# Performance work log

Measured on AMD Instinct MI355X. Metric: run time of the kernel, lower is better.

The kernel has to match this reference:

```python
import jax, jax.numpy as jnp
import numpy as np

B, T, D, HS = 8, 2048, 768, 64  # batch, seq, n_embd, head_size


def setup_inputs() -> dict:
    key = jax.random.key(0)
    kx, kq, kk, kv = jax.random.split(key, 4)
    scale = 1.0 / np.sqrt(D)
    return {
        "x": jax.random.normal(kx, (B, T, D), dtype=jnp.float32),
        "Wq": jax.random.normal(kq, (D, HS), dtype=jnp.float32) * scale,
        "Wk": jax.random.normal(kk, (D, HS), dtype=jnp.float32) * scale,
        "Wv": jax.random.normal(kv, (D, HS), dtype=jnp.float32) * scale,
    }


def reference(x, Wq, Wk, Wv):
    # q,k,v: [B,T,HS]
    q = jnp.einsum("btd,dh->bth", x, Wq)
    k = jnp.einsum("btd,dh->bth", x, Wk)
    v = jnp.einsum("btd,dh->bth", x, Wv)
    hs = k.shape[-1]
    # scaled scores: [B,T,T]
    wei = jnp.einsum("bth,bsh->bts", q, k) * (hs ** -0.5)
    # causal mask (lower-triangular keeps, upper -> -inf)
    causal = jnp.tril(jnp.ones((x.shape[1], x.shape[1]), dtype=bool))
    wei = jnp.where(causal[None, :, :], wei, -jnp.inf)
    wei = jax.nn.softmax(wei, axis=-1)
    return jnp.einsum("bts,bsh->bth", wei, v)
```

## Files before the change

kernel.cpp:

```cpp
#include <hip/hip_runtime.h>

typedef float  f32x4  __attribute__((ext_vector_type(4)));
typedef short  short8 __attribute__((ext_vector_type(8)));
typedef short  short4_ __attribute__((ext_vector_type(4)));

constexpr int Bb = 8, T = 2048, D = 768, HS = 64;
constexpr int BT = Bb * T;
constexpr int QT = T / 64;
constexpr int PSTRIDE = 64 * 64 + 128;

__device__ __forceinline__ short f2bf(float f) {
    unsigned u = __builtin_bit_cast(unsigned, f);
    unsigned r = (u + 0x7FFFu + ((u >> 16) & 1u)) >> 16;
    return (short)r;
}

__device__ __forceinline__ void gld_lds16(const short* g, short* l) {
    __builtin_amdgcn_global_load_lds(
        (const __attribute__((address_space(1))) unsigned int*)g,
        (__attribute__((address_space(3))) unsigned int*)l, 16, 0, 0);
}

__global__ __launch_bounds__(256) void wt_kernel(const float* __restrict__ Wq,
                                                 const float* __restrict__ Wk,
                                                 const float* __restrict__ Wv,
                                                 short* __restrict__ Wt) {
    int n = blockIdx.x;
    const float* W = (n < 64) ? Wq : (n < 128) ? Wk : Wv;
    int c = n & 63;
    for (int kk = threadIdx.x; kk < D; kk += 256)
        Wt[n * D + kk] = f2bf(W[kk * HS + c]);
}

__global__ __launch_bounds__(512) void qkv_proj(const float* __restrict__ x,
                                                const short* __restrict__ Wt,
                                                short* __restrict__ qws,
                                                short* __restrict__ kws,
                                                short* __restrict__ vtg) {
    __shared__ alignas(16) short xs[2][64 * 72];
    __shared__ alignas(16) short wtile[2][192 * 64];

    const int tid  = threadIdx.x;
    const int lane = tid & 63, w = tid >> 6;
    const int lo   = lane & 15, hi = lane >> 4;
    const int wr   = w >> 2, wc = w & 3;
    const int row0 = blockIdx.x * 64;
    const int b    = row0 >> 11, t0 = row0 & 2047;

    const int xr0 = tid >> 4, xsg = tid & 15;
    const float* xsrc0 = &x[(size_t)(row0 + xr0) * D + xsg * 4];
    const float* xsrc1 = &x[(size_t)(row0 + 32 + xr0) * D + xsg * 4];

    f32x4 acc[6];
#pragma unroll
    for (int j = 0; j < 6; j++) acc[j] = f32x4{0.f, 0.f, 0.f, 0.f};

#define STAGE(bb, kc)                                                          \
    {                                                                          \
        _Pragma("unroll")                                                      \
        for (int it = 0; it < 3; it++) {                                       \
            int ci = it * 512 + w * 64 + lane;                                 \
            int n = ci >> 3, seg = ci & 7;                                     \
            gld_lds16(&Wt[(size_t)n * D + (kc) * 64 + ((seg ^ (n & 7)) << 3)], \
                      &wtile[bb][(it * 512 + w * 64) * 8]);                    \
        }                                                                      \
        float4 f0 = *reinterpret_cast<const float4*>(xsrc0 + (kc) * 64);       \
        float4 f1 = *reinterpret_cast<const float4*>(xsrc1 + (kc) * 64);       \
        short4_ h0, h1;                                                        \
        h0[0] = f2bf(f0.x); h0[1] = f2bf(f0.y); h0[2] = f2bf(f0.z); h0[3] = f2bf(f0.w); \
        h1[0] = f2bf(f1.x); h1[1] = f2bf(f1.y); h1[2] = f2bf(f1.z); h1[3] = f2bf(f1.w); \
        *reinterpret_cast<short4_*>(&xs[bb][xr0 * 72 + xsg * 4]) = h0;         \
        *reinterpret_cast<short4_*>(&xs[bb][(32 + xr0) * 72 + xsg * 4]) = h1;  \
    }

    STAGE(0, 0);
    __syncthreads();

    for (int kc = 0; kc < 12; kc++) {
        const int bb = kc & 1;
        if (kc + 1 < 12) STAGE(bb ^ 1, kc + 1);

#pragma unroll
        for (int m = 0; m < 2; m++) {
            const int ar = (wr * 32 + m * 16 + lo) * 72;
            short8 a0 = *reinterpret_cast<const short8*>(&xs[bb][ar + hi * 8]);
            short8 a1 = *reinterpret_cast<const short8*>(&xs[bb][ar + 32 + hi * 8]);
#pragma unroll
            for (int j = 0; j < 3; j++) {
                const int row = wc * 48 + j * 16 + lo;
                const int rx  = (row & 7) << 3;
                short8 b0 = *reinterpret_cast<const short8*>(
                    &wtile[bb][row * 64 + ((hi << 3) ^ rx)]);
                short8 b1 = *reinterpret_cast<const short8*>(
                    &wtile[bb][row * 64 + (((hi + 4) << 3) ^ rx)]);
                acc[m * 3 + j] = __builtin_amdgcn_mfma_f32_16x16x32_bf16(a0, b0, acc[m * 3 + j], 0, 0, 0);
                acc[m * 3 + j] = __builtin_amdgcn_mfma_f32_16x16x32_bf16(a1, b1, acc[m * 3 + j], 0, 0, 0);
            }
        }
        __syncthreads();
    }
#undef STAGE

#pragma unroll
    for (int m = 0; m < 2; m++) {
        const int orow = row0 + wr * 32 + m * 16 + hi * 4;
#pragma unroll
        for (int j = 0; j < 3; j++) {
            const int cb = wc * 48 + j * 16;
            const f32x4 a = acc[m * 3 + j];
            if (cb < 64) {
#pragma unroll
                for (int r = 0; r < 4; r++)
                    qws[(size_t)(orow + r) * HS + cb + lo] = f2bf(a[r] * 0.125f);
            } else if (cb < 128) {
#pragma unroll
                for (int r = 0; r < 4; r++)
                    kws[(size_t)(orow + r) * HS + cb - 64 + lo] = f2bf(a[r]);
            } else {
                short4_ pv;
#pragma unroll
                for (int r = 0; r < 4; r++) pv[r] = f2bf(a[r]);
                *reinterpret_cast<short4_*>(
                    &vtg[((size_t)b * 64 + cb - 128 + lo) * T + t0 + wr * 32 + m * 16 + hi * 4]) = pv;
            }
        }
    }
}

__global__ __launch_bounds__(256) void attn(const short* __restrict__ qg,
                                            const short* __restrict__ kg,
                                            const short* __restrict__ vtg,
                                            float* __restrict__ part, int S) {
    __shared__ short ks[2][64 * 64];
    __shared__ short vts[2][64 * 64];
    __shared__ short ps[4][16 * 64];

    const int tid  = threadIdx.x;
    const int lane = tid & 63, w = tid >> 6;
    const int lo   = lane & 15, hi = lane >> 4;
    const int bid  = blockIdx.x;
    const int per_b = QT * S;
    const int b    = bid / per_b;
    const int r2   = bid % per_b;
    const int qt   = 31 - (r2 / S);
    const int c    = r2 % S;
    const int nkt  = qt + 1;
    const int base = nkt / S, rem = nkt % S;
    const int niter = base + (c < rem ? 1 : 0);
    const int kt0   = c * base + (c < rem ? c : rem);
    float* pout = part + (size_t)((b * QT + qt) * S + c) * PSTRIDE;

    float m_[4], l_[4];
    f32x4 oacc[4];
#pragma unroll
    for (int r = 0; r < 4; r++) { m_[r] = -1e30f; l_[r] = 0.0f; }
#pragma unroll
    for (int i = 0; i < 4; i++) oacc[i] = f32x4{0.f, 0.f, 0.f, 0.f};

    if (niter > 0) {
        const int qrow = qt * 64 + w * 16 + lo;
        const size_t qbase = ((size_t)b * T + qrow) * HS;
        short8 qa0 = *reinterpret_cast<const short8*>(&qg[qbase + hi * 8]);
        short8 qa1 = *reinterpret_cast<const short8*>(&qg[qbase + 32 + hi * 8]);

        const int srow = tid >> 2, scs = tid & 3, r7 = srow & 7;
        const int w0 = srow * 64 + (((scs * 2)     ^ r7) << 3);
        const int w1 = srow * 64 + (((scs * 2 + 1) ^ r7) << 3);
        const size_t kgoff = (size_t)b * T * HS;
        const size_t vgoff = ((size_t)b * 64 + srow) * T;

        short8 ka, kb2, va, vb;
        {
            const short* kp = &kg[kgoff + (size_t)(kt0 * 64 + srow) * HS + scs * 16];
            ka = *reinterpret_cast<const short8*>(kp);
            kb2 = *reinterpret_cast<const short8*>(kp + 8);
            const short* vp = &vtg[vgoff + kt0 * 64 + scs * 16];
            va = *reinterpret_cast<const short8*>(vp);
            vb = *reinterpret_cast<const short8*>(vp + 8);
        }
        *reinterpret_cast<short8*>(&ks[0][w0])  = ka;
        *reinterpret_cast<short8*>(&ks[0][w1])  = kb2;
        *reinterpret_cast<short8*>(&vts[0][w0]) = va;
        *reinterpret_cast<short8*>(&vts[0][w1]) = vb;

        int cur = 0;
        for (int i = 0; i < niter; i++) {
            const int kt = kt0 + i;
            if (i + 1 < niter) {
                const short* kp = &kg[kgoff + (size_t)((kt + 1) * 64 + srow) * HS + scs * 16];
                ka = *reinterpret_cast<const short8*>(kp);
                kb2 = *reinterpret_cast<const short8*>(kp + 8);
                const short* vp = &vtg[vgoff + (kt + 1) * 64 + scs * 16];
                va = *reinterpret_cast<const short8*>(vp);
                vb = *reinterpret_cast<const short8*>(vp + 8);
            }
            __syncthreads();

            f32x4 sacc[4];
#pragma unroll
            for (int nt = 0; nt < 4; nt++) sacc[nt] = f32x4{0.f, 0.f, 0.f, 0.f};
            __builtin_amdgcn_s_setprio(1);
#pragma unroll
            for (int nt = 0; nt < 4; nt++) {
                const int row = nt * 16 + lo, rr = row & 7;
                short8 b0 = *reinterpret_cast<const short8*>(
                    &ks[cur][row * 64 + ((hi ^ rr) << 3)]);
                short8 b1 = *reinterpret_cast<const short8*>(
                    &ks[cur][row * 64 + (((hi + 4) ^ rr) << 3)]);
                sacc[nt] = __builtin_amdgcn_mfma_f32_16x16x32_bf16(qa0, b0, sacc[nt], 0, 0, 0);
                sacc[nt] = __builtin_amdgcn_mfma_f32_16x16x32_bf16(qa1, b1, sacc[nt], 0, 0, 0);
            }
            __builtin_amdgcn_s_setprio(0);

            if (kt == qt) {
#pragma unroll
                for (int nt = 0; nt < 4; nt++)
#pragma unroll
                    for (int r = 0; r < 4; r++)
                        if (nt * 16 + lo > w * 16 + hi * 4 + r) sacc[nt][r] = -1e30f;
            }

#pragma unroll
            for (int r = 0; r < 4; r++) {
                float t0m = fmaxf(fmaxf(sacc[0][r], sacc[1][r]),
                                  fmaxf(sacc[2][r], sacc[3][r]));
#pragma unroll
                for (int off = 1; off < 16; off <<= 1) t0m = fmaxf(t0m, __shfl_xor(t0m, off));
                float mnew = fmaxf(m_[r], t0m);
                float corr = __expf(m_[r] - mnew);
                float psum = 0.0f;
#pragma unroll
                for (int nt = 0; nt < 4; nt++) {
                    float p = __expf(sacc[nt][r] - mnew);
                    sacc[nt][r] = p;
                    psum += p;
                }
#pragma unroll
                for (int off = 1; off < 16; off <<= 1) psum += __shfl_xor(psum, off);
                l_[r] = l_[r] * corr + psum;
                m_[r] = mnew;
#pragma unroll
                for (int nt = 0; nt < 4; nt++) oacc[nt][r] *= corr;
            }

#pragma unroll
            for (int nt = 0; nt < 4; nt++)
#pragma unroll
                for (int r = 0; r < 4; r++) {
                    const int qr = hi * 4 + r;
                    const int seg = nt * 2 + (lo >> 3);
                    ps[w][qr * 64 + ((seg ^ (qr & 7)) << 3) + (lo & 7)] = f2bf(sacc[nt][r]);
                }

            const int pl7 = lo & 7;
            short8 pa0 = *reinterpret_cast<const short8*>(
                &ps[w][lo * 64 + ((hi ^ pl7) << 3)]);
            short8 pa1 = *reinterpret_cast<const short8*>(
                &ps[w][lo * 64 + (((hi + 4) ^ pl7) << 3)]);
            __builtin_amdgcn_s_setprio(1);
#pragma unroll
            for (int nt = 0; nt < 4; nt++) {
                const int row = nt * 16 + lo, rr = row & 7;
                short8 b0 = *reinterpret_cast<const short8*>(
                    &vts[cur][row * 64 + ((hi ^ rr) << 3)]);
                short8 b1 = *reinterpret_cast<const short8*>(
                    &vts[cur][row * 64 + (((hi + 4) ^ rr) << 3)]);
                oacc[nt] = __builtin_amdgcn_mfma_f32_16x16x32_bf16(pa0, b0, oacc[nt], 0, 0, 0);
                oacc[nt] = __builtin_amdgcn_mfma_f32_16x16x32_bf16(pa1, b1, oacc[nt], 0, 0, 0);
            }
            __builtin_amdgcn_s_setprio(0);

            if (i + 1 < niter) {
                *reinterpret_cast<short8*>(&ks[cur ^ 1][w0])  = ka;
                *reinterpret_cast<short8*>(&ks[cur ^ 1][w1])  = kb2;
                *reinterpret_cast<short8*>(&vts[cur ^ 1][w0]) = va;
                *reinterpret_cast<short8*>(&vts[cur ^ 1][w1]) = vb;
            }
            cur ^= 1;
        }
    }

#pragma unroll
    for (int nt = 0; nt < 4; nt++)
#pragma unroll
        for (int r = 0; r < 4; r++)
            pout[(w * 16 + hi * 4 + r) * 64 + nt * 16 + lo] = oacc[nt][r];
    if (lo == 0) {
#pragma unroll
        for (int r = 0; r < 4; r++) {
            const int row = w * 16 + hi * 4 + r;
            pout[4096 + row] = m_[r];
            pout[4160 + row] = l_[r];
        }
    }
}

__global__ __launch_bounds__(256) void combine(const float* __restrict__ part,
                                               float* __restrict__ out, int S) {
    const int bid = blockIdx.x;
    const int b = bid >> 5, qt = bid & 31;
    const float* p = part + (size_t)bid * S * PSTRIDE;
    const int row = threadIdx.x >> 2, cs = threadIdx.x & 3;

    float mv[4], lv[4], av[4];
    float M = -1e30f;
    for (int s = 0; s < S; s++) {
        mv[s] = p[(size_t)s * PSTRIDE + 4096 + row];
        lv[s] = p[(size_t)s * PSTRIDE + 4160 + row];
        M = fmaxf(M, mv[s]);
    }
    float den = 0.0f;
    for (int s = 0; s < S; s++) { av[s] = __expf(mv[s] - M); den += lv[s] * av[s]; }
    float inv = 1.0f / den;

    float* o = out + ((size_t)b * T + qt * 64 + row) * HS + cs * 16;
#pragma unroll
    for (int i = 0; i < 4; i++) {
        float4 res = make_float4(0.f, 0.f, 0.f, 0.f);
        for (int s = 0; s < S; s++) {
            float4 v = *reinterpret_cast<const float4*>(
                p + (size_t)s * PSTRIDE + row * 64 + cs * 16 + i * 4);
            res.x += v.x * av[s]; res.y += v.y * av[s];
            res.z += v.z * av[s]; res.w += v.w * av[s];
        }
        res.x *= inv; res.y *= inv; res.z *= inv; res.w *= inv;
        *reinterpret_cast<float4*>(o + i * 4) = res;
    }
}

extern "C" void kernel_launch(void* const* d_in, const int* in_sizes, int n_in,
                              void* d_out, int out_size, void* d_ws, size_t ws_size,
                              hipStream_t stream) {
    const float* x  = (const float*)d_in[0];
    const float* Wq = (const float*)d_in[1];
    const float* Wk = (const float*)d_in[2];
    const float* Wv = (const float*)d_in[3];
    float* out = (float*)d_out;

    short* ws   = (short*)d_ws;
    short* qws  = ws;
    short* kws  = qws + (size_t)BT * HS;
    short* vtws = kws + (size_t)BT * HS;
    short* Wt   = vtws + (size_t)BT * HS;
    float* part = (float*)(Wt + (size_t)192 * D);

    const size_t fixed = (size_t)3 * BT * HS * 2 + (size_t)192 * D * 2;
    int S = 4;
    while (S > 1 && fixed + (size_t)Bb * QT * S * PSTRIDE * 4 > ws_size) S >>= 1;

    wt_kernel<<<192, 256, 0, stream>>>(Wq, Wk, Wv, Wt);
    qkv_proj<<<BT / 64, 512, 0, stream>>>(x, Wt, qws, kws, vtws);
    attn<<<Bb * QT * S, 256, 0, stream>>>(qws, kws, vtws, part, S);
    combine<<<Bb * QT, 256, 0, stream>>>(part, out, S);
}
```

Baseline: 63.42 us.

## Halve QKV projection row tile and load x directly into registers

The QKV projection block now covers 32 rows instead of 64, which doubles the grid. Each wave loads its x fragment straight from global memory into registers, with a one-step prefetch, and converts it to bf16 there, so the shared-memory x tile is gone. A launch-bounds occupancy hint is added. The aim is more parallelism and less LDS traffic in the projection. In exchange, each W tile loaded into LDS is reused across half as many rows, so total W traffic doubles.

```diff
diff --git a/kernel.cpp b/kernel.cpp
--- a/kernel.cpp
+++ b/kernel.cpp
@@ -32,30 +32,27 @@
         Wt[n * D + kk] = f2bf(W[kk * HS + c]);
 }
 
-__global__ __launch_bounds__(512) void qkv_proj(const float* __restrict__ x,
-                                                const short* __restrict__ Wt,
-                                                short* __restrict__ qws,
-                                                short* __restrict__ kws,
-                                                short* __restrict__ vtg) {
-    __shared__ alignas(16) short xs[2][64 * 72];
+__global__ __launch_bounds__(512, 4) void qkv_proj(const float* __restrict__ x,
+                                                   const short* __restrict__ Wt,
+                                                   short* __restrict__ qws,
+                                                   short* __restrict__ kws,
+                                                   short* __restrict__ vtg) {
     __shared__ alignas(16) short wtile[2][192 * 64];
 
     const int tid  = threadIdx.x;
     const int lane = tid & 63, w = tid >> 6;
     const int lo   = lane & 15, hi = lane >> 4;
     const int wr   = w >> 2, wc = w & 3;
-    const int row0 = blockIdx.x * 64;
+    const int row0 = blockIdx.x * 32;
     const int b    = row0 >> 11, t0 = row0 & 2047;
 
-    const int xr0 = tid >> 4, xsg = tid & 15;
-    const float* xsrc0 = &x[(size_t)(row0 + xr0) * D + xsg * 4];
-    const float* xsrc1 = &x[(size_t)(row0 + 32 + xr0) * D + xsg * 4];
-
-    f32x4 acc[6];
-#pragma unroll
-    for (int j = 0; j < 6; j++) acc[j] = f32x4{0.f, 0.f, 0.f, 0.f};
-
-#define STAGE(bb, kc)                                                          \
+    const float* xrow = &x[(size_t)(row0 + wr * 16 + lo) * D];
+
+    f32x4 acc[3];
+#pragma unroll
+    for (int j = 0; j < 3; j++) acc[j] = f32x4{0.f, 0.f, 0.f, 0.f};
+
+#define STAGE_W(bb, kc)                                                        \
     {                                                                          \
         _Pragma("unroll")                                                      \
         for (int it = 0; it < 3; it++) {                                       \
@@ -64,65 +61,74 @@
             gld_lds16(&Wt[(size_t)n * D + (kc) * 64 + ((seg ^ (n & 7)) << 3)], \
                       &wtile[bb][(it * 512 + w * 64) * 8]);                    \
         }                                                                      \
-        float4 f0 = *reinterpret_cast<const float4*>(xsrc0 + (kc) * 64);       \
-        float4 f1 = *reinterpret_cast<const float4*>(xsrc1 + (kc) * 64);       \
-        short4_ h0, h1;                                                        \
-        h0[0] = f2bf(f0.x); h0[1] = f2bf(f0.y); h0[2] = f2bf(f0.z); h0[3] = f2bf(f0.w); \
-        h1[0] = f2bf(f1.x); h1[1] = f2bf(f1.y); h1[2] = f2bf(f1.z); h1[3] = f2bf(f1.w); \
-        *reinterpret_cast<short4_*>(&xs[bb][xr0 * 72 + xsg * 4]) = h0;         \
-        *reinterpret_cast<short4_*>(&xs[bb][(32 + xr0) * 72 + xsg * 4]) = h1;  \
-    }
-
-    STAGE(0, 0);
+    }
+
+    STAGE_W(0, 0);
+    float4 cur[4], nxt[4];
+    cur[0] = *reinterpret_cast<const float4*>(xrow + hi * 8);
+    cur[1] = *reinterpret_cast<const float4*>(xrow + hi * 8 + 4);
+    cur[2] = *reinterpret_cast<const float4*>(xrow + 32 + hi * 8);
+    cur[3] = *reinterpret_cast<const float4*>(xrow + 32 + hi * 8 + 4);
     __syncthreads();
 
+#pragma unroll
     for (int kc = 0; kc < 12; kc++) {
         const int bb = kc & 1;
-        if (kc + 1 < 12) STAGE(bb ^ 1, kc + 1);
-
-#pragma unroll
-        for (int m = 0; m < 2; m++) {
-            const int ar = (wr * 32 + m * 16 + lo) * 72;
-            short8 a0 = *reinterpret_cast<const short8*>(&xs[bb][ar + hi * 8]);
-            short8 a1 = *reinterpret_cast<const short8*>(&xs[bb][ar + 32 + hi * 8]);
-#pragma unroll
-            for (int j = 0; j < 3; j++) {
-                const int row = wc * 48 + j * 16 + lo;
-                const int rx  = (row & 7) << 3;
-                short8 b0 = *reinterpret_cast<const short8*>(
-                    &wtile[bb][row * 64 + ((hi << 3) ^ rx)]);
-                short8 b1 = *reinterpret_cast<const short8*>(
-                    &wtile[bb][row * 64 + (((hi + 4) << 3) ^ rx)]);
-                acc[m * 3 + j] = __builtin_amdgcn_mfma_f32_16x16x32_bf16(a0, b0, acc[m * 3 + j], 0, 0, 0);
-                acc[m * 3 + j] = __builtin_amdgcn_mfma_f32_16x16x32_bf16(a1, b1, acc[m * 3 + j], 0, 0, 0);
-            }
+        if (kc + 1 < 12) {
+            STAGE_W(bb ^ 1, kc + 1);
+            const float* xp = xrow + (kc + 1) * 64;
+            nxt[0] = *reinterpret_cast<const float4*>(xp + hi * 8);
+            nxt[1] = *reinterpret_cast<const float4*>(xp + hi * 8 + 4);
+            nxt[2] = *reinterpret_cast<const float4*>(xp + 32 + hi * 8);
+            nxt[3] = *reinterpret_cast<const float4*>(xp + 32 + hi * 8 + 4);
+        }
+
+        short8 a0, a1;
+#pragma unroll
+        for (int e = 0; e < 4; e++) {
+            a0[e]     = f2bf(cur[0][e]);
+            a0[e + 4] = f2bf(cur[1][e]);
+            a1[e]     = f2bf(cur[2][e]);
+            a1[e + 4] = f2bf(cur[3][e]);
+        }
+
+#pragma unroll
+        for (int j = 0; j < 3; j++) {
+            const int row = wc * 48 + j * 16 + lo;
+            const int rx  = (row & 7) << 3;
+            short8 b0 = *reinterpret_cast<const short8*>(
+                &wtile[bb][row * 64 + ((hi << 3) ^ rx)]);
+            short8 b1 = *reinterpret_cast<const short8*>(
+                &wtile[bb][row * 64 + (((hi + 4) << 3) ^ rx)]);
+            acc[j] = __builtin_amdgcn_mfma_f32_16x16x32_bf16(a0, b0, acc[j], 0, 0, 0);
+            acc[j] = __builtin_amdgcn_mfma_f32_16x16x32_bf16(a1, b1, acc[j], 0, 0, 0);
         }
         __syncthreads();
-    }
-#undef STAGE
-
-#pragma unroll
-    for (int m = 0; m < 2; m++) {
-        const int orow = row0 + wr * 32 + m * 16 + hi * 4;
-#pragma unroll
-        for (int j = 0; j < 3; j++) {
-            const int cb = wc * 48 + j * 16;
-            const f32x4 a = acc[m * 3 + j];
-            if (cb < 64) {
-#pragma unroll
-                for (int r = 0; r < 4; r++)
-                    qws[(size_t)(orow + r) * HS + cb + lo] = f2bf(a[r] * 0.125f);
-            } else if (cb < 128) {
-#pragma unroll
-                for (int r = 0; r < 4; r++)
-                    kws[(size_t)(orow + r) * HS + cb - 64 + lo] = f2bf(a[r]);
-            } else {
-                short4_ pv;
-#pragma unroll
-                for (int r = 0; r < 4; r++) pv[r] = f2bf(a[r]);
-                *reinterpret_cast<short4_*>(
-                    &vtg[((size_t)b * 64 + cb - 128 + lo) * T + t0 + wr * 32 + m * 16 + hi * 4]) = pv;
-            }
+
+#pragma unroll
+        for (int i = 0; i < 4; i++) cur[i] = nxt[i];
+    }
+#undef STAGE_W
+
+    const int orow = row0 + wr * 16 + hi * 4;
+#pragma unroll
+    for (int j = 0; j < 3; j++) {
+        const int cb = wc * 48 + j * 16;
+        const f32x4 a = acc[j];
+        if (cb < 64) {
+#pragma unroll
+            for (int r = 0; r < 4; r++)
+                qws[(size_t)(orow + r) * HS + cb + lo] = f2bf(a[r] * 0.125f);
+        } else if (cb < 128) {
+#pragma unroll
+            for (int r = 0; r < 4; r++)
+                kws[(size_t)(orow + r) * HS + cb - 64 + lo] = f2bf(a[r]);
+        } else {
+            short4_ pv;
+#pragma unroll
+            for (int r = 0; r < 4; r++) pv[r] = f2bf(a[r]);
+            *reinterpret_cast<short4_*>(
+                &vtg[((size_t)b * 64 + cb - 128 + lo) * T + t0 + wr * 16 + hi * 4]) = pv;
         }
     }
 }
@@ -349,7 +355,7 @@
     while (S > 1 && fixed + (size_t)Bb * QT * S * PSTRIDE * 4 > ws_size) S >>= 1;
 
     wt_kernel<<<192, 256, 0, stream>>>(Wq, Wk, Wv, Wt);
-    qkv_proj<<<BT / 64, 512, 0, stream>>>(x, Wt, qws, kws, vtws);
+    qkv_proj<<<BT / 32, 512, 0, stream>>>(x, Wt, qws, kws, vtws);
     attn<<<Bb * QT * S, 256, 0, stream>>>(qws, kws, vtws, part, S);
     combine<<<Bb * QT, 256, 0, stream>>>(part, out, S);
 }
```

New measurement: 75.43 us. +18.9%, slower.

## Process two key tiles per attention iteration and stage V transpose through LDS

Applied to the files above, without the earlier changes.

The attention loop now handles two 64-key tiles per iteration, with double-buffered LDS holding both tiles. This halves the number of block barriers and online-softmax rescale steps per key, and shares one max and sum reduction across 128 keys. Separately, the QKV projection writes V into shared memory and then stores the transposed V with coalesced 16-byte writes instead of scattered 8-byte writes. The trade-off is double the LDS footprint and more registers in attention, which may lower occupancy.

```diff
diff --git a/kernel.cpp b/kernel.cpp
--- a/kernel.cpp
+++ b/kernel.cpp
@@ -39,6 +39,7 @@
                                                 short* __restrict__ vtg) {
     __shared__ alignas(16) short xs[2][64 * 72];
     __shared__ alignas(16) short wtile[2][192 * 64];
+    __shared__ alignas(16) short vs[64 * 72];
 
     const int tid  = threadIdx.x;
     const int lane = tid & 63, w = tid >> 6;
@@ -104,6 +105,7 @@
 #pragma unroll
     for (int m = 0; m < 2; m++) {
         const int orow = row0 + wr * 32 + m * 16 + hi * 4;
+        const int trow = wr * 32 + m * 16 + hi * 4;
 #pragma unroll
         for (int j = 0; j < 3; j++) {
             const int cb = wc * 48 + j * 16;
@@ -117,13 +119,20 @@
                 for (int r = 0; r < 4; r++)
                     kws[(size_t)(orow + r) * HS + cb - 64 + lo] = f2bf(a[r]);
             } else {
-                short4_ pv;
-#pragma unroll
-                for (int r = 0; r < 4; r++) pv[r] = f2bf(a[r]);
-                *reinterpret_cast<short4_*>(
-                    &vtg[((size_t)b * 64 + cb - 128 + lo) * T + t0 + wr * 32 + m * 16 + hi * 4]) = pv;
+#pragma unroll
+                for (int r = 0; r < 4; r++)
+                    vs[(trow + r) * 72 + cb - 128 + lo] = f2bf(a[r]);
             }
         }
+    }
+    __syncthreads();
+    {
+        const int h = tid >> 3, ts = tid & 7;
+        short8 tmp;
+#pragma unroll
+        for (int e = 0; e < 8; e++) tmp[e] = vs[(ts * 8 + e) * 72 + h];
+        *reinterpret_cast<short8*>(
+            &vtg[((size_t)b * 64 + h) * T + t0 + ts * 8]) = tmp;
     }
 }
 
@@ -131,9 +140,9 @@
                                             const short* __restrict__ kg,
                                             const short* __restrict__ vtg,
                                             float* __restrict__ part, int S) {
-    __shared__ short ks[2][64 * 64];
-    __shared__ short vts[2][64 * 64];
-    __shared__ short ps[4][16 * 64];
+    __shared__ short ks[2][2][64 * 64];
+    __shared__ short vts[2][2][64 * 64];
+    __shared__ short ps[4][16 * 128];
 
     const int tid  = threadIdx.x;
     const int lane = tid & 63, w = tid >> 6;
@@ -169,71 +178,112 @@
         const size_t kgoff = (size_t)b * T * HS;
         const size_t vgoff = ((size_t)b * 64 + srow) * T;
 
-        short8 ka, kb2, va, vb;
-        {
-            const short* kp = &kg[kgoff + (size_t)(kt0 * 64 + srow) * HS + scs * 16];
-            ka = *reinterpret_cast<const short8*>(kp);
-            kb2 = *reinterpret_cast<const short8*>(kp + 8);
-            const short* vp = &vtg[vgoff + kt0 * 64 + scs * 16];
-            va = *reinterpret_cast<const short8*>(vp);
-            vb = *reinterpret_cast<const short8*>(vp + 8);
-        }
-        *reinterpret_cast<short8*>(&ks[0][w0])  = ka;
-        *reinterpret_cast<short8*>(&ks[0][w1])  = kb2;
-        *reinterpret_cast<short8*>(&vts[0][w0]) = va;
-        *reinterpret_cast<short8*>(&vts[0][w1]) = vb;
-
+#define LOADT(kt64, KA, KB, VA, VB)                                            \
+    {                                                                          \
+        const short* kp = &kg[kgoff + (size_t)((kt64) * 64 + srow) * HS + scs * 16]; \
+        KA = *reinterpret_cast<const short8*>(kp);                             \
+        KB = *reinterpret_cast<const short8*>(kp + 8);                         \
+        const short* vp = &vtg[vgoff + (kt64) * 64 + scs * 16];                \
+        VA = *reinterpret_cast<const short8*>(vp);                             \
+        VB = *reinterpret_cast<const short8*>(vp + 8);                         \
+    }
+#define STORET(buf, half, KA, KB, VA, VB)                                      \
+    {                                                                          \
+        *reinterpret_cast<short8*>(&ks[buf][half][w0])  = KA;                  \
+        *reinterpret_cast<short8*>(&ks[buf][half][w1])  = KB;                  \
+        *reinterpret_cast<short8*>(&vts[buf][half][w0]) = VA;                  \
+        *reinterpret_cast<short8*>(&vts[buf][half][w1]) = VB;                  \
+    }
+
+        short8 kA0, kB0, vA0, vB0, kA1, kB1, vA1, vB1;
+        LOADT(kt0, kA0, kB0, vA0, vB0);
+        if (1 < niter) LOADT(kt0 + 1, kA1, kB1, vA1, vB1);
+        STORET(0, 0, kA0, kB0, vA0, vB0);
+        if (1 < niter) STORET(0, 1, kA1, kB1, vA1, vB1);
+
+        const int npair = (niter + 1) >> 1;
         int cur = 0;
-        for (int i = 0; i < niter; i++) {
-            const int kt = kt0 + i;
-            if (i + 1 < niter) {
-                const short* kp = &kg[kgoff + (size_t)((kt + 1) * 64 + srow) * HS + scs * 16];
-                ka = *reinterpret_cast<const short8*>(kp);
-                kb2 = *reinterpret_cast<const short8*>(kp + 8);
-                const short* vp = &vtg[vgoff + (kt + 1) * 64 + scs * 16];
-                va = *reinterpret_cast<const short8*>(vp);
-                vb = *reinterpret_cast<const short8*>(vp + 8);
+        for (int ii = 0; ii < npair; ii++) {
+            const int ta = kt0 + 2 * ii;
+            const bool hasB = (2 * ii + 1) < niter;
+            const bool pf   = (ii + 1) < npair;
+            const bool pfB  = (2 * ii + 3) < niter;
+            if (pf) {
+                LOADT(ta + 2, kA0, kB0, vA0, vB0);
+                if (pfB) LOADT(ta + 3, kA1, kB1, vA1, vB1);
             }
             __syncthreads();
 
-            f32x4 sacc[4];
-#pragma unroll
-            for (int nt = 0; nt < 4; nt++) sacc[nt] = f32x4{0.f, 0.f, 0.f, 0.f};
+            f32x4 sa[4], sb[4];
+#pragma unroll
+            for (int nt = 0; nt < 4; nt++) sa[nt] = f32x4{0.f, 0.f, 0.f, 0.f};
             __builtin_amdgcn_s_setprio(1);
 #pragma unroll
             for (int nt = 0; nt < 4; nt++) {
-                const int row = nt * 16 + lo, rr = row & 7;
+                const int row = nt * 16 + lo, rr = (row & 7) << 3;
                 short8 b0 = *reinterpret_cast<const short8*>(
-                    &ks[cur][row * 64 + ((hi ^ rr) << 3)]);
+                    &ks[cur][0][row * 64 + ((hi << 3) ^ rr)]);
                 short8 b1 = *reinterpret_cast<const short8*>(
-                    &ks[cur][row * 64 + (((hi + 4) ^ rr) << 3)]);
-                sacc[nt] = __builtin_amdgcn_mfma_f32_16x16x32_bf16(qa0, b0, sacc[nt], 0, 0, 0);
-                sacc[nt] = __builtin_amdgcn_mfma_f32_16x16x32_bf16(qa1, b1, sacc[nt], 0, 0, 0);
+                    &ks[cur][0][row * 64 + (((hi + 4) << 3) ^ rr)]);
+                sa[nt] = __builtin_amdgcn_mfma_f32_16x16x32_bf16(qa0, b0, sa[nt], 0, 0, 0);
+                sa[nt] = __builtin_amdgcn_mfma_f32_16x16x32_bf16(qa1, b1, sa[nt], 0, 0, 0);
+            }
+            if (hasB) {
+#pragma unroll
+                for (int nt = 0; nt < 4; nt++) sb[nt] = f32x4{0.f, 0.f, 0.f, 0.f};
+#pragma unroll
+                for (int nt = 0; nt < 4; nt++) {
+                    const int row = nt * 16 + lo, rr = (row & 7) << 3;
+                    short8 b0 = *reinterpret_cast<const short8*>(
+                        &ks[cur][1][row * 64 + ((hi << 3) ^ rr)]);
+                    short8 b1 = *reinterpret_cast<const short8*>(
+                        &ks[cur][1][row * 64 + (((hi + 4) << 3) ^ rr)]);
+                    sb[nt] = __builtin_amdgcn_mfma_f32_16x16x32_bf16(qa0, b0, sb[nt], 0, 0, 0);
+                    sb[nt] = __builtin_amdgcn_mfma_f32_16x16x32_bf16(qa1, b1, sb[nt], 0, 0, 0);
+                }
             }
             __builtin_amdgcn_s_setprio(0);
 
-            if (kt == qt) {
+            if (ta == qt) {
 #pragma unroll
                 for (int nt = 0; nt < 4; nt++)
 #pragma unroll
                     for (int r = 0; r < 4; r++)
-                        if (nt * 16 + lo > w * 16 + hi * 4 + r) sacc[nt][r] = -1e30f;
+                        if (nt * 16 + lo > w * 16 + hi * 4 + r) sa[nt][r] = -1e30f;
+            }
+            if (hasB && ta + 1 == qt) {
+#pragma unroll
+                for (int nt = 0; nt < 4; nt++)
+#pragma unroll
+                    for (int r = 0; r < 4; r++)
+                        if (nt * 16 + lo > w * 16 + hi * 4 + r) sb[nt][r] = -1e30f;
             }
 
 #pragma unroll
             for (int r = 0; r < 4; r++) {
-                float t0m = fmaxf(fmaxf(sacc[0][r], sacc[1][r]),
-                                  fmaxf(sacc[2][r], sacc[3][r]));
-#pragma unroll
-                for (int off = 1; off < 16; off <<= 1) t0m = fmaxf(t0m, __shfl_xor(t0m, off));
-                float mnew = fmaxf(m_[r], t0m);
+                float tm = fmaxf(fmaxf(sa[0][r], sa[1][r]),
+                                 fmaxf(sa[2][r], sa[3][r]));
+                if (hasB)
+                    tm = fmaxf(tm, fmaxf(fmaxf(sb[0][r], sb[1][r]),
+                                         fmaxf(sb[2][r], sb[3][r])));
+#pragma unroll
+                for (int off = 1; off < 16; off <<= 1) tm = fmaxf(tm, __shfl_xor(tm, off));
+                float mnew = fmaxf(m_[r], tm);
                 float corr = __expf(m_[r] - mnew);
                 float psum = 0.0f;
 #pragma unroll
                 for (int nt = 0; nt < 4; nt++) {
-                    float p = __expf(sacc[nt][r] - mnew);
-                    sacc[nt][r] = p;
+                    float p = __expf(sa[nt][r] - mnew);
+                    sa[nt][r] = p;
                     psum += p;
+                }
+                if (hasB) {
+#pragma unroll
+                    for (int nt = 0; nt < 4; nt++) {
+                        float p = __expf(sb[nt][r] - mnew);
+                        sb[nt][r] = p;
+                        psum += p;
+                    }
                 }
 #pragma unroll
                 for (int off = 1; off < 16; off <<= 1) psum += __shfl_xor(psum, off);
@@ -249,35 +299,63 @@
                 for (int r = 0; r < 4; r++) {
                     const int qr = hi * 4 + r;
                     const int seg = nt * 2 + (lo >> 3);
-                    ps[w][qr * 64 + ((seg ^ (qr & 7)) << 3) + (lo & 7)] = f2bf(sacc[nt][r]);
+                    ps[w][qr * 128 + ((seg ^ (qr & 7)) << 3) + (lo & 7)] = f2bf(sa[nt][r]);
                 }
+            if (hasB) {
+#pragma unroll
+                for (int nt = 0; nt < 4; nt++)
+#pragma unroll
+                    for (int r = 0; r < 4; r++) {
+                        const int qr = hi * 4 + r;
+                        const int seg = 8 + nt * 2 + (lo >> 3);
+                        ps[w][qr * 128 + ((seg ^ (qr & 7)) << 3) + (lo & 7)] = f2bf(sb[nt][r]);
+                    }
+            }
 
             const int pl7 = lo & 7;
             short8 pa0 = *reinterpret_cast<const short8*>(
-                &ps[w][lo * 64 + ((hi ^ pl7) << 3)]);
+                &ps[w][lo * 128 + ((hi ^ pl7) << 3)]);
             short8 pa1 = *reinterpret_cast<const short8*>(
-                &ps[w][lo * 64 + (((hi + 4) ^ pl7) << 3)]);
+                &ps[w][lo * 128 + (((hi + 4) ^ pl7) << 3)]);
             __builtin_amdgcn_s_setprio(1);
 #pragma unroll
             for (int nt = 0; nt < 4; nt++) {
-                const int row = nt * 16 + lo, rr = row & 7;
+                const int row = nt * 16 + lo, rr = (row & 7) << 3;
                 short8 b0 = *reinterpret_cast<const short8*>(
-                    &vts[cur][row * 64 + ((hi ^ rr) << 3)]);
+                    &vts[cur][0][row * 64 + ((hi << 3) ^ rr)]);
                 short8 b1 = *reinterpret_cast<const short8*>(
-                    &vts[cur][row * 64 + (((hi + 4) ^ rr) << 3)]);
+                    &vts[cur][0][row * 64 + (((hi + 4) << 3) ^ rr)]);
                 oacc[nt] = __builtin_amdgcn_mfma_f32_16x16x32_bf16(pa0, b0, oacc[nt], 0, 0, 0);
                 oacc[nt] = __builtin_amdgcn_mfma_f32_16x16x32_bf16(pa1, b1, oacc[nt], 0, 0, 0);
             }
             __builtin_amdgcn_s_setprio(0);
-
-            if (i + 1 < niter) {
-                *reinterpret_cast<short8*>(&ks[cur ^ 1][w0])  = ka;
-                *reinterpret_cast<short8*>(&ks[cur ^ 1][w1])  = kb2;
-                *reinterpret_cast<short8*>(&vts[cur ^ 1][w0]) = va;
-                *reinterpret_cast<short8*>(&vts[cur ^ 1][w1]) = vb;
+            if (hasB) {
+                short8 pa2 = *reinterpret_cast<const short8*>(
+                    &ps[w][lo * 128 + (((hi + 8) ^ pl7) << 3)]);
+                short8 pa3 = *reinterpret_cast<const short8*>(
+                    &ps[w][lo * 128 + (((hi + 12) ^ pl7) << 3)]);
+                __builtin_amdgcn_s_setprio(1);
+#pragma unroll
+                for (int nt = 0; nt < 4; nt++) {
+                    const int row = nt * 16 + lo, rr = (row & 7) << 3;
+                    short8 b0 = *reinterpret_cast<const short8*>(
+                        &vts[cur][1][row * 64 + ((hi << 3) ^ rr)]);
+                    short8 b1 = *reinterpret_cast<const short8*>(
+                        &vts[cur][1][row * 64 + (((hi + 4) << 3) ^ rr)]);
+                    oacc[nt] = __builtin_amdgcn_mfma_f32_16x16x32_bf16(pa2, b0, oacc[nt], 0, 0, 0);
+                    oacc[nt] = __builtin_amdgcn_mfma_f32_16x16x32_bf16(pa3, b1, oacc[nt], 0, 0, 0);
+                }
+                __builtin_amdgcn_s_setprio(0);
+            }
+
+            if (pf) {
+                STORET(cur ^ 1, 0, kA0, kB0, vA0, vB0);
+                if (pfB) STORET(cur ^ 1, 1, kA1, kB1, vA1, vB1);
             }
             cur ^= 1;
         }
+#undef LOADT
+#undef STORET
     }
 
 #pragma unroll
```

Measured after the change: 66.60 us. 1.05x slower.

## Transpose QK^T MFMA so each lane owns a query row, add lazy rescaling

Applied to the files above, without the earlier changes.

Swaps the MFMA operand order so the score accumulator is transposed: each lane holds one query row across keys. Row max now needs only two cross-lane shuffles instead of four per row, and the running max/sum become scalars per lane. A lazy rescale skips the output correction unless some row's max grows by more than 8, and launch bounds request 4 blocks per SIMD. The P tile is written to LDS with a new XOR swizzle. The risks are extra shuffles to broadcast corrections, possible register pressure under the occupancy hint, and the bounded-growth threshold affecting numerics.

```diff
diff --git a/kernel.cpp b/kernel.cpp
--- a/kernel.cpp
+++ b/kernel.cpp
@@ -127,10 +127,10 @@
     }
 }
 
-__global__ __launch_bounds__(256) void attn(const short* __restrict__ qg,
-                                            const short* __restrict__ kg,
-                                            const short* __restrict__ vtg,
-                                            float* __restrict__ part, int S) {
+__global__ __launch_bounds__(256, 4) void attn(const short* __restrict__ qg,
+                                               const short* __restrict__ kg,
+                                               const short* __restrict__ vtg,
+                                               float* __restrict__ part, int S) {
     __shared__ short ks[2][64 * 64];
     __shared__ short vts[2][64 * 64];
     __shared__ short ps[4][16 * 64];
@@ -150,10 +150,8 @@
     const int kt0   = c * base + (c < rem ? c : rem);
     float* pout = part + (size_t)((b * QT + qt) * S + c) * PSTRIDE;
 
-    float m_[4], l_[4];
+    float m_ = -1e30f, l_ = 0.0f;
     f32x4 oacc[4];
-#pragma unroll
-    for (int r = 0; r < 4; r++) { m_[r] = -1e30f; l_[r] = 0.0f; }
 #pragma unroll
     for (int i = 0; i < 4; i++) oacc[i] = f32x4{0.f, 0.f, 0.f, 0.f};
 
@@ -183,6 +181,7 @@
         *reinterpret_cast<short8*>(&vts[0][w0]) = va;
         *reinterpret_cast<short8*>(&vts[0][w1]) = vb;
 
+        const int pswz = (lo & 7) << 3;
         int cur = 0;
         for (int i = 0; i < niter; i++) {
             const int kt = kt0 + i;
@@ -207,8 +206,8 @@
                     &ks[cur][row * 64 + ((hi ^ rr) << 3)]);
                 short8 b1 = *reinterpret_cast<const short8*>(
                     &ks[cur][row * 64 + (((hi + 4) ^ rr) << 3)]);
-                sacc[nt] = __builtin_amdgcn_mfma_f32_16x16x32_bf16(qa0, b0, sacc[nt], 0, 0, 0);
-                sacc[nt] = __builtin_amdgcn_mfma_f32_16x16x32_bf16(qa1, b1, sacc[nt], 0, 0, 0);
+                sacc[nt] = __builtin_amdgcn_mfma_f32_16x16x32_bf16(b0, qa0, sacc[nt], 0, 0, 0);
+                sacc[nt] = __builtin_amdgcn_mfma_f32_16x16x32_bf16(b1, qa1, sacc[nt], 0, 0, 0);
             }
             __builtin_amdgcn_s_setprio(0);
 
@@ -217,46 +216,43 @@
                 for (int nt = 0; nt < 4; nt++)
 #pragma unroll
                     for (int r = 0; r < 4; r++)
-                        if (nt * 16 + lo > w * 16 + hi * 4 + r) sacc[nt][r] = -1e30f;
-            }
-
-#pragma unroll
-            for (int r = 0; r < 4; r++) {
-                float t0m = fmaxf(fmaxf(sacc[0][r], sacc[1][r]),
-                                  fmaxf(sacc[2][r], sacc[3][r]));
-#pragma unroll
-                for (int off = 1; off < 16; off <<= 1) t0m = fmaxf(t0m, __shfl_xor(t0m, off));
-                float mnew = fmaxf(m_[r], t0m);
-                float corr = __expf(m_[r] - mnew);
-                float psum = 0.0f;
-#pragma unroll
-                for (int nt = 0; nt < 4; nt++) {
-                    float p = __expf(sacc[nt][r] - mnew);
-                    sacc[nt][r] = p;
-                    psum += p;
+                        if (nt * 16 + hi * 4 + r > w * 16 + lo) sacc[nt][r] = -1e30f;
+            }
+
+            float tm = fmaxf(fmaxf(fmaxf(sacc[0][0], sacc[0][1]), fmaxf(sacc[0][2], sacc[0][3])),
+                             fmaxf(fmaxf(sacc[1][0], sacc[1][1]), fmaxf(sacc[1][2], sacc[1][3])));
+            tm = fmaxf(tm, fmaxf(fmaxf(fmaxf(sacc[2][0], sacc[2][1]), fmaxf(sacc[2][2], sacc[2][3])),
+                                 fmaxf(fmaxf(sacc[3][0], sacc[3][1]), fmaxf(sacc[3][2], sacc[3][3]))));
+            tm = fmaxf(tm, __shfl_xor(tm, 16));
+            tm = fmaxf(tm, __shfl_xor(tm, 32));
+
+            if (!__all(tm <= m_ + 8.0f)) {
+                float mnew = fmaxf(m_, tm);
+                float corr = __expf(m_ - mnew);
+                l_ *= corr;
+#pragma unroll
+                for (int r = 0; r < 4; r++) {
+                    float cr = __shfl(corr, (lane & 48) | (hi * 4 + r));
+#pragma unroll
+                    for (int nt = 0; nt < 4; nt++) oacc[nt][r] *= cr;
                 }
-#pragma unroll
-                for (int off = 1; off < 16; off <<= 1) psum += __shfl_xor(psum, off);
-                l_[r] = l_[r] * corr + psum;
-                m_[r] = mnew;
-#pragma unroll
-                for (int nt = 0; nt < 4; nt++) oacc[nt][r] *= corr;
+                m_ = mnew;
             }
 
 #pragma unroll
             for (int nt = 0; nt < 4; nt++)
 #pragma unroll
                 for (int r = 0; r < 4; r++) {
-                    const int qr = hi * 4 + r;
-                    const int seg = nt * 2 + (lo >> 3);
-                    ps[w][qr * 64 + ((seg ^ (qr & 7)) << 3) + (lo & 7)] = f2bf(sacc[nt][r]);
+                    float p = __expf(sacc[nt][r] - m_);
+                    l_ += p;
+                    const int key = nt * 16 + hi * 4 + r;
+                    ps[w][lo * 64 + (key ^ pswz)] = f2bf(p);
                 }
 
-            const int pl7 = lo & 7;
             short8 pa0 = *reinterpret_cast<const short8*>(
-                &ps[w][lo * 64 + ((hi ^ pl7) << 3)]);
+                &ps[w][lo * 64 + ((hi << 3) ^ pswz)]);
             short8 pa1 = *reinterpret_cast<const short8*>(
-                &ps[w][lo * 64 + (((hi + 4) ^ pl7) << 3)]);
+                &ps[w][lo * 64 + (((hi + 4) << 3) ^ pswz)]);
             __builtin_amdgcn_s_setprio(1);
 #pragma unroll
             for (int nt = 0; nt < 4; nt++) {
@@ -280,17 +276,27 @@
         }
     }
 
+    float lt = l_;
+    lt += __shfl_xor(lt, 16);
+    lt += __shfl_xor(lt, 32);
+
 #pragma unroll
     for (int nt = 0; nt < 4; nt++)
 #pragma unroll
         for (int r = 0; r < 4; r++)
             pout[(w * 16 + hi * 4 + r) * 64 + nt * 16 + lo] = oacc[nt][r];
+    float mfor[4], lfor[4];
+#pragma unroll
+    for (int r = 0; r < 4; r++) {
+        mfor[r] = __shfl(m_, (lane & 48) | (hi * 4 + r));
+        lfor[r] = __shfl(lt, (lane & 48) | (hi * 4 + r));
+    }
     if (lo == 0) {
 #pragma unroll
         for (int r = 0; r < 4; r++) {
             const int row = w * 16 + hi * 4 + r;
-            pout[4096 + row] = m_[r];
-            pout[4160 + row] = l_[r];
+            pout[4096 + row] = mfor[r];
+            pout[4160 + row] = lfor[r];
         }
     }
 }
```

After: 56.24 us. 11.3% less time.
